# Performance work log

Hardware: AMD Instinct MI355X
Metric: run time of the kernel (lower is better)

## Reference

```python
import jax, jax.numpy as jnp
import numpy as np

B, M = 4, 8192
NUM_PAD = 1024  # trailing pc columns zeroed to exercise the zero-column mask


def setup_inputs() -> dict:
    key = jax.random.key(0)
    k1, k2 = jax.random.split(key)
    vertices = jax.random.normal(k1, (B, 3, 128, 64), dtype=jnp.float32)
    pc = jax.random.normal(k2, (B, 3, M), dtype=jnp.float32)
    # zero-pad some columns: the original filters columns where all 3 coords == 0
    pc = pc.at[:, :, M - NUM_PAD:].set(0.0)
    return {"vertices": vertices, "pc": pc}


def reference(vertices, pc):
    b = vertices.shape[0]
    v = vertices.reshape(b, 3, -1).transpose(0, 2, 1)   # [B, N, 3] mesh vertices
    p = pc.transpose(0, 2, 1)                           # [B, M, 3] point cloud
    valid = ~jnp.all(pc == 0.0, axis=1)                 # [B, M] non-zero columns
    # squared pairwise distances pc -> vertices: [B, M, N]
    d2 = (
        jnp.sum(p * p, axis=-1)[:, :, None]
        + jnp.sum(v * v, axis=-1)[:, None, :]
        - 2.0 * jnp.einsum("bmd,bnd->bmn", p, v)
    )
    dist2 = jnp.min(d2, axis=-1)                        # [B, M] NN sq-dist per pc point
    valid_f = valid.astype(dist2.dtype)
    per_item = jnp.sum(dist2 * valid_f, axis=-1) / jnp.sum(valid_f, axis=-1)  # mean over valid points
    return jnp.mean(per_item)
```

## Files before the change

### kernel.cpp

```cpp
#include <hip/hip_runtime.h>

#define MPTS 8192
#define NVERT 8192
#define BQ 512
#define VC 512
#define TPB 256

__device__ __forceinline__ unsigned int enc_f32(float f) {
    unsigned int b = __float_as_uint(f);
    return (b & 0x80000000u) ? ~b : (b | 0x80000000u);
}
__device__ __forceinline__ float dec_f32(unsigned int e) {
    unsigned int b = (e & 0x80000000u) ? (e & 0x7FFFFFFFu) : ~e;
    return __uint_as_float(b);
}

__global__ __launch_bounds__(TPB) void minpart_kernel(
        const float* __restrict__ vert,
        const float* __restrict__ pc,
        unsigned int* __restrict__ wsmin)
{
    __shared__ float4 lv[VC];
    const int b     = blockIdx.z;
    const int vbase = blockIdx.y * VC;
    const int mbase = blockIdx.x * BQ;
    const int tid   = threadIdx.x;

    const float* pcb = pc + (size_t)b * 3 * MPTS;
    const int m0 = mbase + tid;
    const int m1 = mbase + tid + TPB;
    const float p0x = pcb[m0],        p0y = pcb[MPTS + m0],  p0z = pcb[2 * MPTS + m0];
    const float p1x = pcb[m1],        p1y = pcb[MPTS + m1],  p1z = pcb[2 * MPTS + m1];
    const float n0x = -2.0f * p0x, n0y = -2.0f * p0y, n0z = -2.0f * p0z;
    const float n1x = -2.0f * p1x, n1y = -2.0f * p1y, n1z = -2.0f * p1z;

    const float* vb = vert + (size_t)b * 3 * NVERT + vbase;
    for (int i = tid; i < VC; i += TPB) {
        float vx = vb[i], vy = vb[NVERT + i], vz = vb[2 * NVERT + i];
        lv[i] = make_float4(vx, vy, vz, vx * vx + vy * vy + vz * vz);
    }
    __syncthreads();

    float t0a = 1e30f, t0b = 1e30f, t1a = 1e30f, t1b = 1e30f;
    #pragma unroll 4
    for (int i = 0; i < VC; i += 2) {
        const float4 va = lv[i];
        const float4 vbv = lv[i + 1];
        t0a = fminf(t0a, fmaf(n0x, va.x,  fmaf(n0y, va.y,  fmaf(n0z, va.z,  va.w))));
        t1a = fminf(t1a, fmaf(n1x, va.x,  fmaf(n1y, va.y,  fmaf(n1z, va.z,  va.w))));
        t0b = fminf(t0b, fmaf(n0x, vbv.x, fmaf(n0y, vbv.y, fmaf(n0z, vbv.z, vbv.w))));
        t1b = fminf(t1b, fmaf(n1x, vbv.x, fmaf(n1y, vbv.y, fmaf(n1z, vbv.z, vbv.w))));
    }
    const float t0 = fminf(t0a, t0b);
    const float t1 = fminf(t1a, t1b);
    atomicMin(&wsmin[(size_t)b * MPTS + m0], enc_f32(t0));
    atomicMin(&wsmin[(size_t)b * MPTS + m1], enc_f32(t1));
}

__global__ __launch_bounds__(1024) void reduce_kernel(
        const float* __restrict__ pc,
        const unsigned int* __restrict__ wsmin,
        float* __restrict__ out, int B)
{
    const int tid = threadIdx.x;
    const int b   = tid >> 8;
    const int r   = tid & 255;

    float sum = 0.0f, cnt = 0.0f;
    if (b < B) {
        const float* pcb = pc + (size_t)b * 3 * MPTS;
        for (int k = 0; k < MPTS; k += 256) {
            const int m = r + k;
            const float px = pcb[m], py = pcb[MPTS + m], pz = pcb[2 * MPTS + m];
            const bool valid = !(px == 0.0f && py == 0.0f && pz == 0.0f);
            const float t = dec_f32(wsmin[(size_t)b * MPTS + m]);
            const float d2 = fmaf(px, px, fmaf(py, py, fmaf(pz, pz, t)));
            if (valid) { sum += d2; cnt += 1.0f; }
        }
    }
    for (int off = 32; off > 0; off >>= 1) {
        sum += __shfl_down(sum, off);
        cnt += __shfl_down(cnt, off);
    }
    __shared__ float ssum[16], scnt[16];
    const int wid = tid >> 6, lane = tid & 63;
    if (lane == 0) { ssum[wid] = sum; scnt[wid] = cnt; }
    __syncthreads();
    if (tid == 0) {
        float acc = 0.0f;
        for (int g = 0; g < B; ++g) {
            const float s = ssum[g * 4] + ssum[g * 4 + 1] + ssum[g * 4 + 2] + ssum[g * 4 + 3];
            const float c = scnt[g * 4] + scnt[g * 4 + 1] + scnt[g * 4 + 2] + scnt[g * 4 + 3];
            acc += s / c;
        }
        out[0] = acc / (float)B;
    }
}

extern "C" void kernel_launch(void* const* d_in, const int* in_sizes, int n_in,
                              void* d_out, int out_size, void* d_ws, size_t ws_size,
                              hipStream_t stream) {
    const float* vert = (const float*)d_in[0];
    const float* pc   = (const float*)d_in[1];
    float* out        = (float*)d_out;
    const int B = in_sizes[0] / (3 * NVERT);

    unsigned int* wsmin = (unsigned int*)d_ws;
    hipMemsetAsync(wsmin, 0xFF, (size_t)B * MPTS * sizeof(unsigned int), stream);

    dim3 grid(MPTS / BQ, NVERT / VC, B);
    minpart_kernel<<<grid, TPB, 0, stream>>>(vert, pc, wsmin);
    reduce_kernel<<<1, 1024, 0, stream>>>(pc, wsmin, out, B);
}
```

Baseline: 86.46 us.

## Use packed fp32 math, 4 points per thread, and parallel two-stage reduction

The min-distance kernel now processes four query points per thread and computes two vertices at once with 2-wide vector FMA/min, intended to map to packed fp32 instructions and halve issue count per FLOP. Vertex data in LDS is split into two float4 arrays holding pairs of vertices, so each LDS read is reused across more points. The single-block final reduction becomes a 32-block partial reduction plus a tiny final kernel, spreading the reduction across CUs at the cost of an extra launch. Grid size in the M dimension halves, which lowers the block count and may reduce occupancy.

```diff
diff --git a/kernel.cpp b/kernel.cpp
--- a/kernel.cpp
+++ b/kernel.cpp
@@ -1,16 +1,19 @@
 #include <hip/hip_runtime.h>
+
+typedef float v2f __attribute__((ext_vector_type(2)));
 
 #define MPTS 8192
 #define NVERT 8192
-#define BQ 512
+#define TPB 256
+#define PPT 4
+#define BQ (TPB*PPT)
 #define VC 512
-#define TPB 256
 
-__device__ __forceinline__ unsigned int enc_f32(float f) {
+static __device__ __forceinline__ unsigned int enc_f32(float f) {
     unsigned int b = __float_as_uint(f);
     return (b & 0x80000000u) ? ~b : (b | 0x80000000u);
 }
-__device__ __forceinline__ float dec_f32(unsigned int e) {
+static __device__ __forceinline__ float dec_f32(unsigned int e) {
     unsigned int b = (e & 0x80000000u) ? (e & 0x7FFFFFFFu) : ~e;
     return __uint_as_float(b);
 }
@@ -20,81 +23,107 @@
         const float* __restrict__ pc,
         unsigned int* __restrict__ wsmin)
 {
-    __shared__ float4 lv[VC];
-    const int b     = blockIdx.z;
-    const int vbase = blockIdx.y * VC;
-    const int mbase = blockIdx.x * BQ;
-    const int tid   = threadIdx.x;
+    __shared__ float4 lvA[VC / 2];
+    __shared__ float4 lvB[VC / 2];
+    const int b = blockIdx.z, vbase = blockIdx.y * VC, mbase = blockIdx.x * BQ;
+    const int tid = threadIdx.x;
 
     const float* pcb = pc + (size_t)b * 3 * MPTS;
-    const int m0 = mbase + tid;
-    const int m1 = mbase + tid + TPB;
-    const float p0x = pcb[m0],        p0y = pcb[MPTS + m0],  p0z = pcb[2 * MPTS + m0];
-    const float p1x = pcb[m1],        p1y = pcb[MPTS + m1],  p1z = pcb[2 * MPTS + m1];
-    const float n0x = -2.0f * p0x, n0y = -2.0f * p0y, n0z = -2.0f * p0z;
-    const float n1x = -2.0f * p1x, n1y = -2.0f * p1y, n1z = -2.0f * p1z;
+    v2f npx[PPT], npy[PPT], npz[PPT];
+    int mm[PPT];
+    #pragma unroll
+    for (int p = 0; p < PPT; ++p) {
+        const int m = mbase + tid + p * TPB;
+        mm[p] = m;
+        const float x = pcb[m], y = pcb[MPTS + m], z = pcb[2 * MPTS + m];
+        npx[p] = (v2f){-2.0f * x, -2.0f * x};
+        npy[p] = (v2f){-2.0f * y, -2.0f * y};
+        npz[p] = (v2f){-2.0f * z, -2.0f * z};
+    }
 
     const float* vb = vert + (size_t)b * 3 * NVERT + vbase;
-    for (int i = tid; i < VC; i += TPB) {
-        float vx = vb[i], vy = vb[NVERT + i], vz = vb[2 * NVERT + i];
-        lv[i] = make_float4(vx, vy, vz, vx * vx + vy * vy + vz * vz);
+    const v2f* vbx = (const v2f*)(vb);
+    const v2f* vby = (const v2f*)(vb + NVERT);
+    const v2f* vbz = (const v2f*)(vb + 2 * NVERT);
+    for (int i = tid; i < VC / 2; i += TPB) {
+        const v2f x = vbx[i], y = vby[i], z = vbz[i];
+        const v2f w = x * x + y * y + z * z;
+        lvA[i] = make_float4(x.x, x.y, y.x, y.y);
+        lvB[i] = make_float4(z.x, z.y, w.x, w.y);
     }
     __syncthreads();
 
-    float t0a = 1e30f, t0b = 1e30f, t1a = 1e30f, t1b = 1e30f;
+    v2f acc[PPT];
+    #pragma unroll
+    for (int p = 0; p < PPT; ++p) acc[p] = (v2f){1e30f, 1e30f};
+
     #pragma unroll 4
-    for (int i = 0; i < VC; i += 2) {
-        const float4 va = lv[i];
-        const float4 vbv = lv[i + 1];
-        t0a = fminf(t0a, fmaf(n0x, va.x,  fmaf(n0y, va.y,  fmaf(n0z, va.z,  va.w))));
-        t1a = fminf(t1a, fmaf(n1x, va.x,  fmaf(n1y, va.y,  fmaf(n1z, va.z,  va.w))));
-        t0b = fminf(t0b, fmaf(n0x, vbv.x, fmaf(n0y, vbv.y, fmaf(n0z, vbv.z, vbv.w))));
-        t1b = fminf(t1b, fmaf(n1x, vbv.x, fmaf(n1y, vbv.y, fmaf(n1z, vbv.z, vbv.w))));
+    for (int j = 0; j < VC / 2; ++j) {
+        const float4 A = lvA[j], Bv = lvB[j];
+        const v2f vx = {A.x, A.y}, vy = {A.z, A.w};
+        const v2f vz = {Bv.x, Bv.y}, vw = {Bv.z, Bv.w};
+        #pragma unroll
+        for (int p = 0; p < PPT; ++p) {
+            const v2f t = __builtin_elementwise_fma(npx[p], vx,
+                           __builtin_elementwise_fma(npy[p], vy,
+                            __builtin_elementwise_fma(npz[p], vz, vw)));
+            acc[p] = __builtin_elementwise_min(acc[p], t);
+        }
     }
-    const float t0 = fminf(t0a, t0b);
-    const float t1 = fminf(t1a, t1b);
-    atomicMin(&wsmin[(size_t)b * MPTS + m0], enc_f32(t0));
-    atomicMin(&wsmin[(size_t)b * MPTS + m1], enc_f32(t1));
+
+    unsigned int* wm = wsmin + (size_t)b * MPTS;
+    #pragma unroll
+    for (int p = 0; p < PPT; ++p)
+        atomicMin(&wm[mm[p]], enc_f32(fminf(acc[p].x, acc[p].y)));
 }
 
-__global__ __launch_bounds__(1024) void reduce_kernel(
+__global__ __launch_bounds__(256) void reduce_kernel(
         const float* __restrict__ pc,
         const unsigned int* __restrict__ wsmin,
-        float* __restrict__ out, int B)
+        v2f* __restrict__ part)
 {
+    const int b = blockIdx.x >> 3, sl = blockIdx.x & 7;
     const int tid = threadIdx.x;
-    const int b   = tid >> 8;
-    const int r   = tid & 255;
+    const float* pcb = pc + (size_t)b * 3 * MPTS;
+    const unsigned int* wm = wsmin + (size_t)b * MPTS;
 
     float sum = 0.0f, cnt = 0.0f;
-    if (b < B) {
-        const float* pcb = pc + (size_t)b * 3 * MPTS;
-        for (int k = 0; k < MPTS; k += 256) {
-            const int m = r + k;
-            const float px = pcb[m], py = pcb[MPTS + m], pz = pcb[2 * MPTS + m];
-            const bool valid = !(px == 0.0f && py == 0.0f && pz == 0.0f);
-            const float t = dec_f32(wsmin[(size_t)b * MPTS + m]);
-            const float d2 = fmaf(px, px, fmaf(py, py, fmaf(pz, pz, t)));
-            if (valid) { sum += d2; cnt += 1.0f; }
-        }
+    #pragma unroll
+    for (int k = 0; k < 4; ++k) {
+        const int m = sl * 1024 + k * 256 + tid;
+        const float x = pcb[m], y = pcb[MPTS + m], z = pcb[2 * MPTS + m];
+        const float t = dec_f32(wm[m]);
+        const float d2 = fmaf(x, x, fmaf(y, y, fmaf(z, z, t)));
+        if (!(x == 0.0f && y == 0.0f && z == 0.0f)) { sum += d2; cnt += 1.0f; }
     }
-    for (int off = 32; off > 0; off >>= 1) {
+    for (int off = 32; off; off >>= 1) {
         sum += __shfl_down(sum, off);
         cnt += __shfl_down(cnt, off);
     }
-    __shared__ float ssum[16], scnt[16];
+    __shared__ float ss[4], sc[4];
     const int wid = tid >> 6, lane = tid & 63;
-    if (lane == 0) { ssum[wid] = sum; scnt[wid] = cnt; }
+    if (lane == 0) { ss[wid] = sum; sc[wid] = cnt; }
     __syncthreads();
-    if (tid == 0) {
-        float acc = 0.0f;
-        for (int g = 0; g < B; ++g) {
-            const float s = ssum[g * 4] + ssum[g * 4 + 1] + ssum[g * 4 + 2] + ssum[g * 4 + 3];
-            const float c = scnt[g * 4] + scnt[g * 4 + 1] + scnt[g * 4 + 2] + scnt[g * 4 + 3];
-            acc += s / c;
-        }
-        out[0] = acc / (float)B;
+    if (tid == 0)
+        part[blockIdx.x] = (v2f){ss[0] + ss[1] + ss[2] + ss[3],
+                                 sc[0] + sc[1] + sc[2] + sc[3]};
+}
+
+__global__ __launch_bounds__(64) void final_kernel(
+        const v2f* __restrict__ part, float* __restrict__ out, int B)
+{
+    const int lane = threadIdx.x;
+    float s = 0.0f, c = 0.0f;
+    if (lane < B * 8) { const v2f p = part[lane]; s = p.x; c = p.y; }
+    #pragma unroll
+    for (int off = 4; off; off >>= 1) {
+        s += __shfl_down(s, off);
+        c += __shfl_down(c, off);
     }
+    const float r = s / c;
+    float acc = 0.0f;
+    for (int g = 0; g < B; ++g) acc += __shfl(r, g * 8);
+    if (lane == 0) out[0] = acc / (float)B;
 }
 
 extern "C" void kernel_launch(void* const* d_in, const int* in_sizes, int n_in,
@@ -106,9 +135,11 @@
     const int B = in_sizes[0] / (3 * NVERT);
 
     unsigned int* wsmin = (unsigned int*)d_ws;
+    v2f* part = (v2f*)(wsmin + (size_t)B * MPTS);
     hipMemsetAsync(wsmin, 0xFF, (size_t)B * MPTS * sizeof(unsigned int), stream);
 
     dim3 grid(MPTS / BQ, NVERT / VC, B);
     minpart_kernel<<<grid, TPB, 0, stream>>>(vert, pc, wsmin);
-    reduce_kernel<<<1, 1024, 0, stream>>>(pc, wsmin, out, B);
+    reduce_kernel<<<B * 8, 256, 0, stream>>>(pc, wsmin, part);
+    final_kernel<<<1, 64, 0, stream>>>(part, out, B);
 }
```

Result: faster. 78.30 us (-9.4%).
